# Kernel optimization log

Hardware: AMD Instinct MI355X
Metric: run time of the kernel (lower is better)

Reference implementation:

```python
import jax, jax.numpy as jnp
import numpy as np

N = 262144
H = 512
NUM_SEGMENTS = 64

def setup_inputs() -> dict:
    key = jax.random.key(0)
    k1, k2, k3, k4 = jax.random.split(key, 4)
    h_V = jax.random.normal(k1, (N, H), dtype=jnp.float32)
    batch_id = jnp.sort(jax.random.randint(k2, (N,), 0, NUM_SEGMENTS))
    scale = 1.0 / np.sqrt(H)
    W1 = jax.random.normal(k3, (H, H), dtype=jnp.float32) * scale
    b1 = jnp.zeros((H,), dtype=jnp.float32)
    W2 = jax.random.normal(k4, (H, H), dtype=jnp.float32) * scale
    b2 = jnp.zeros((H,), dtype=jnp.float32)
    return {"h_V": h_V, "batch_id": batch_id, "W1": W1, "b1": b1, "W2": W2, "b2": b2}

def reference(h_V, batch_id, W1, b1, W2, b2):
    # scatter_mean over segments: [S, H]
    seg_sum = jax.ops.segment_sum(h_V, batch_id, num_segments=NUM_SEGMENTS)
    counts = jax.ops.segment_sum(jnp.ones((h_V.shape[0],), h_V.dtype), batch_id,
                                 num_segments=NUM_SEGMENTS)
    c_V = seg_sum / jnp.maximum(counts, 1.0)[:, None]
    # gated MLP on per-segment context (nn.Linear: x @ W.T + b)
    hdn = jax.nn.relu(c_V @ W1.T + b1)
    gate = jax.nn.sigmoid(hdn @ W2.T + b2)  # [S, H]
    # gather back to nodes and gate
    return h_V * gate[batch_id]
```

## Files before the change

### kernel.cpp

```cpp
#include <hip/hip_runtime.h>

#define H 512
#define NSEG 64
#define CHUNK 256

__global__ __launch_bounds__(512) void k_segsum(
    const float4* __restrict__ hv, const int* __restrict__ bid,
    float* __restrict__ seg_sum, int* __restrict__ counts)
{
    __shared__ int sb[CHUNK];
    const int base = blockIdx.x * CHUNK;
    const int tid  = threadIdx.x;
    if (tid < CHUNK) sb[tid] = bid[base + tid];
    __syncthreads();

    const int g = tid >> 7;
    const int q = tid & 127;

    float4 acc = make_float4(0.f, 0.f, 0.f, 0.f);
    int cur = sb[g];
    int cnt = 0;

    for (int i = 0; i < CHUNK / 4; ++i) {
        const int rl = g + (i << 2);
        const int s  = sb[rl];
        if (s != cur) {
            float* dst = seg_sum + cur * H + q * 4;
            atomicAdd(dst + 0, acc.x);
            atomicAdd(dst + 1, acc.y);
            atomicAdd(dst + 2, acc.z);
            atomicAdd(dst + 3, acc.w);
            if (q == 0) atomicAdd(counts + cur, cnt);
            acc = make_float4(0.f, 0.f, 0.f, 0.f);
            cnt = 0;
            cur = s;
        }
        const float4 v = hv[(size_t)(base + rl) * (H / 4) + q];
        acc.x += v.x; acc.y += v.y; acc.z += v.z; acc.w += v.w;
        ++cnt;
    }
    float* dst = seg_sum + cur * H + q * 4;
    atomicAdd(dst + 0, acc.x);
    atomicAdd(dst + 1, acc.y);
    atomicAdd(dst + 2, acc.z);
    atomicAdd(dst + 3, acc.w);
    if (q == 0) atomicAdd(counts + cur, cnt);
}

__global__ __launch_bounds__(512) void k_mlp(
    const float* __restrict__ seg_sum, const int* __restrict__ counts,
    const float* __restrict__ W1, const float* __restrict__ b1,
    const float* __restrict__ W2, const float* __restrict__ b2,
    float* __restrict__ gate)
{
    __shared__ float c[H];
    __shared__ float hd[H];
    const int s   = blockIdx.x;
    const int tid = threadIdx.x;

    const float cntf = fmaxf((float)counts[s], 1.0f);
    c[tid] = seg_sum[s * H + tid] / cntf;
    __syncthreads();

    const int w = tid >> 6;
    const int l = tid & 63;

    for (int jb = 0; jb < H / 8; ++jb) {
        const int j = jb * 8 + w;
        const float* __restrict__ wr = W1 + (size_t)j * H;
        float acc = 0.f;
        #pragma unroll
        for (int m = 0; m < H / 64; ++m)
            acc += c[m * 64 + l] * wr[m * 64 + l];
        #pragma unroll
        for (int off = 32; off > 0; off >>= 1)
            acc += __shfl_xor(acc, off, 64);
        if (l == 0) hd[j] = fmaxf(acc + b1[j], 0.f);
    }
    __syncthreads();

    for (int jb = 0; jb < H / 8; ++jb) {
        const int j = jb * 8 + w;
        const float* __restrict__ wr = W2 + (size_t)j * H;
        float acc = 0.f;
        #pragma unroll
        for (int m = 0; m < H / 64; ++m)
            acc += hd[m * 64 + l] * wr[m * 64 + l];
        #pragma unroll
        for (int off = 32; off > 0; off >>= 1)
            acc += __shfl_xor(acc, off, 64);
        if (l == 0) gate[s * H + j] = 1.0f / (1.0f + expf(-(acc + b2[j])));
    }
}

__global__ __launch_bounds__(256) void k_gate(
    const float4* __restrict__ hv, const int* __restrict__ bid,
    const float4* __restrict__ gate, float4* __restrict__ out,
    long long total4)
{
    const long long stride = (long long)gridDim.x * blockDim.x;
    for (long long idx = (long long)blockIdx.x * blockDim.x + threadIdx.x;
         idx < total4; idx += stride) {
        const int row = (int)(idx >> 7);
        const int q   = (int)(idx & 127);
        const int s   = bid[row];
        const float4 v  = hv[idx];
        const float4 gv = gate[(size_t)s * (H / 4) + q];
        out[idx] = make_float4(v.x * gv.x, v.y * gv.y, v.z * gv.z, v.w * gv.w);
    }
}

extern "C" void kernel_launch(void* const* d_in, const int* in_sizes, int n_in,
                              void* d_out, int out_size, void* d_ws, size_t ws_size,
                              hipStream_t stream)
{
    const float* h_V      = (const float*)d_in[0];
    const int*   batch_id = (const int*)d_in[1];
    const float* W1       = (const float*)d_in[2];
    const float* b1       = (const float*)d_in[3];
    const float* W2       = (const float*)d_in[4];
    const float* b2       = (const float*)d_in[5];
    float*       out      = (float*)d_out;

    const int N = in_sizes[0] / H;

    char*  ws       = (char*)d_ws;
    float* seg_sum  = (float*)ws;
    int*   counts   = (int*)(ws + 131072);
    float* gate     = (float*)(ws + 131072 + 256);

    hipMemsetAsync(d_ws, 0, 131072 + 256, stream);

    k_segsum<<<N / CHUNK, 512, 0, stream>>>(
        (const float4*)h_V, batch_id, seg_sum, counts);

    k_mlp<<<NSEG, 512, 0, stream>>>(seg_sum, counts, W1, b1, W2, b2, gate);

    const long long total4 = (long long)N * (H / 4);
    k_gate<<<2048, 256, 0, stream>>>(
        (const float4*)h_V, batch_id, (const float4*)gate, (float4*)out, total4);
}
```

Baseline: 448.8 us.

## Use nontemporal loads/stores and chunked segment-aware gate kernel

Both streaming kernels now use nontemporal vector loads (and stores in the gate kernel) and unroll the row loop by two so two loads are in flight before the segment check. The gate kernel is restructured to match the segsum chunking: each block stages batch ids in shared memory and reloads the gate vector only when the segment changes, instead of a per-element bid and gate lookup in a grid-stride loop. The aim is to cut redundant gathers and cache pollution on the large h_V and output streams. The block count and shape of the gate kernel change as a result.

```diff
diff --git a/kernel.cpp b/kernel.cpp
--- a/kernel.cpp
+++ b/kernel.cpp
@@ -4,8 +4,17 @@
 #define NSEG 64
 #define CHUNK 256
 
+typedef float f4 __attribute__((ext_vector_type(4)));
+
+__device__ __forceinline__ f4 ntload4(const f4* p) {
+    return __builtin_nontemporal_load(p);
+}
+__device__ __forceinline__ void ntstore4(f4* p, f4 v) {
+    __builtin_nontemporal_store(v, p);
+}
+
 __global__ __launch_bounds__(512) void k_segsum(
-    const float4* __restrict__ hv, const int* __restrict__ bid,
+    const f4* __restrict__ hv, const int* __restrict__ bid,
     float* __restrict__ seg_sum, int* __restrict__ counts)
 {
     __shared__ int sb[CHUNK];
@@ -17,33 +26,37 @@
     const int g = tid >> 7;
     const int q = tid & 127;
 
-    float4 acc = make_float4(0.f, 0.f, 0.f, 0.f);
+    f4 acc = (f4)(0.f);
     int cur = sb[g];
     int cnt = 0;
 
-    for (int i = 0; i < CHUNK / 4; ++i) {
-        const int rl = g + (i << 2);
-        const int s  = sb[rl];
-        if (s != cur) {
+    for (int i = 0; i < 64; i += 2) {
+        const int r0 = g + (i << 2);
+        const int r1 = r0 + 4;
+        const f4 v0 = ntload4(hv + (size_t)(base + r0) * (H / 4) + q);
+        const f4 v1 = ntload4(hv + (size_t)(base + r1) * (H / 4) + q);
+        const int s0 = sb[r0];
+        const int s1 = sb[r1];
+        if (s0 != cur) {
             float* dst = seg_sum + cur * H + q * 4;
-            atomicAdd(dst + 0, acc.x);
-            atomicAdd(dst + 1, acc.y);
-            atomicAdd(dst + 2, acc.z);
-            atomicAdd(dst + 3, acc.w);
+            atomicAdd(dst + 0, acc[0]); atomicAdd(dst + 1, acc[1]);
+            atomicAdd(dst + 2, acc[2]); atomicAdd(dst + 3, acc[3]);
             if (q == 0) atomicAdd(counts + cur, cnt);
-            acc = make_float4(0.f, 0.f, 0.f, 0.f);
-            cnt = 0;
-            cur = s;
+            acc = (f4)(0.f); cnt = 0; cur = s0;
         }
-        const float4 v = hv[(size_t)(base + rl) * (H / 4) + q];
-        acc.x += v.x; acc.y += v.y; acc.z += v.z; acc.w += v.w;
-        ++cnt;
+        acc += v0; ++cnt;
+        if (s1 != cur) {
+            float* dst = seg_sum + cur * H + q * 4;
+            atomicAdd(dst + 0, acc[0]); atomicAdd(dst + 1, acc[1]);
+            atomicAdd(dst + 2, acc[2]); atomicAdd(dst + 3, acc[3]);
+            if (q == 0) atomicAdd(counts + cur, cnt);
+            acc = (f4)(0.f); cnt = 0; cur = s1;
+        }
+        acc += v1; ++cnt;
     }
     float* dst = seg_sum + cur * H + q * 4;
-    atomicAdd(dst + 0, acc.x);
-    atomicAdd(dst + 1, acc.y);
-    atomicAdd(dst + 2, acc.z);
-    atomicAdd(dst + 3, acc.w);
+    atomicAdd(dst + 0, acc[0]); atomicAdd(dst + 1, acc[1]);
+    atomicAdd(dst + 2, acc[2]); atomicAdd(dst + 3, acc[3]);
     if (q == 0) atomicAdd(counts + cur, cnt);
 }
 
@@ -93,20 +106,33 @@
     }
 }
 
-__global__ __launch_bounds__(256) void k_gate(
-    const float4* __restrict__ hv, const int* __restrict__ bid,
-    const float4* __restrict__ gate, float4* __restrict__ out,
-    long long total4)
+__global__ __launch_bounds__(512) void k_gate(
+    const f4* __restrict__ hv, const int* __restrict__ bid,
+    const f4* __restrict__ gate, f4* __restrict__ out)
 {
-    const long long stride = (long long)gridDim.x * blockDim.x;
-    for (long long idx = (long long)blockIdx.x * blockDim.x + threadIdx.x;
-         idx < total4; idx += stride) {
-        const int row = (int)(idx >> 7);
-        const int q   = (int)(idx & 127);
-        const int s   = bid[row];
-        const float4 v  = hv[idx];
-        const float4 gv = gate[(size_t)s * (H / 4) + q];
-        out[idx] = make_float4(v.x * gv.x, v.y * gv.y, v.z * gv.z, v.w * gv.w);
+    __shared__ int sb[CHUNK];
+    const int base = blockIdx.x * CHUNK;
+    const int tid  = threadIdx.x;
+    if (tid < CHUNK) sb[tid] = bid[base + tid];
+    __syncthreads();
+
+    const int g = tid >> 7;
+    const int q = tid & 127;
+
+    int cur = sb[g];
+    f4 gv = gate[(size_t)cur * (H / 4) + q];
+
+    for (int i = 0; i < 64; i += 2) {
+        const int r0 = g + (i << 2);
+        const int r1 = r0 + 4;
+        const f4 v0 = ntload4(hv + (size_t)(base + r0) * (H / 4) + q);
+        const f4 v1 = ntload4(hv + (size_t)(base + r1) * (H / 4) + q);
+        const int s0 = sb[r0];
+        const int s1 = sb[r1];
+        if (s0 != cur) { cur = s0; gv = gate[(size_t)cur * (H / 4) + q]; }
+        ntstore4(out + (size_t)(base + r0) * (H / 4) + q, v0 * gv);
+        if (s1 != cur) { cur = s1; gv = gate[(size_t)cur * (H / 4) + q]; }
+        ntstore4(out + (size_t)(base + r1) * (H / 4) + q, v1 * gv);
     }
 }
 
@@ -120,7 +146,6 @@
     const float* b1       = (const float*)d_in[3];
     const float* W2       = (const float*)d_in[4];
     const float* b2       = (const float*)d_in[5];
-    float*       out      = (float*)d_out;
 
     const int N = in_sizes[0] / H;
 
@@ -132,11 +157,10 @@
     hipMemsetAsync(d_ws, 0, 131072 + 256, stream);
 
     k_segsum<<<N / CHUNK, 512, 0, stream>>>(
-        (const float4*)h_V, batch_id, seg_sum, counts);
+        (const f4*)h_V, batch_id, seg_sum, counts);
 
     k_mlp<<<NSEG, 512, 0, stream>>>(seg_sum, counts, W1, b1, W2, b2, gate);
 
-    const long long total4 = (long long)N * (H / 4);
-    k_gate<<<2048, 256, 0, stream>>>(
-        (const float4*)h_V, batch_id, (const float4*)gate, (float4*)out, total4);
+    k_gate<<<N / CHUNK, 512, 0, stream>>>(
+        (const f4*)h_V, batch_id, (const f4*)gate, (f4*)d_out);
 }
```

After: 397.1 us. 1.13x faster.
